# Kernel optimization log

Hardware: AMD Instinct MI355X
Metric: run time of the kernel (lower is better)

Reference implementation:

```python
import jax, jax.numpy as jnp
import numpy as np

B, S, D, H, C = 64, 512, 768, 768, 5


def setup_inputs() -> dict:
    key = jax.random.key(0)
    ks = jax.random.split(key, 7)
    return {
        "hidden_states": jax.random.normal(ks[0], (B, S, D), jnp.float32),
        "mask": jnp.ones((B, S), dtype=bool),
        # Dense(hidden_size, relu)
        "W1": jax.random.normal(ks[1], (D, H), jnp.float32) * 0.02,
        "b1": jnp.zeros((H,), jnp.float32),
        # CRF inner dense -> potentials over num_classes
        "W2": jax.random.normal(ks[2], (H, C), jnp.float32) * 0.02,
        "b2": jnp.zeros((C,), jnp.float32),
        # CRF transition matrix and boundary energies (tfa use_boundary=True)
        "chain_kernel": jax.random.normal(ks[3], (C, C), jnp.float32) * 0.1,
        "left_boundary": jax.random.normal(ks[4], (C,), jnp.float32) * 0.1,
        "right_boundary": jax.random.normal(ks[5], (C,), jnp.float32) * 0.1,
    }


def viterbi_decode(potentials, trans):
    """potentials: [B,S,C], trans: [C,C] -> decoded tags [B,S] int32."""
    pot_t = jnp.swapaxes(potentials, 0, 1)  # [S,B,C]

    def fwd_step(alpha, pot):
        scores = alpha[:, :, None] + trans[None]      # [B,C_prev,C_cur]
        bp = jnp.argmax(scores, axis=1)               # [B,C]
        alpha = jnp.max(scores, axis=1) + pot         # [B,C]
        return alpha, bp

    alpha, bps = jax.lax.scan(fwd_step, pot_t[0], pot_t[1:])  # bps: [S-1,B,C]
    last = jnp.argmax(alpha, axis=-1).astype(jnp.int32)       # [B]

    def back_step(tag, bp):
        prev = jnp.take_along_axis(bp, tag[:, None], axis=1)[:, 0].astype(jnp.int32)
        return prev, prev

    _, tags = jax.lax.scan(back_step, last, bps, reverse=True)  # [S-1,B]
    decoded = jnp.concatenate([jnp.swapaxes(tags, 0, 1), last[:, None]], axis=1)
    return decoded


def reference(hidden_states, mask, W1, b1, W2, b2, chain_kernel,
              left_boundary, right_boundary):
    # Dense + ReLU (dropout is identity at inference / training=False)
    h = jax.nn.relu(jnp.einsum('bsd,dh->bsh', hidden_states, W1) + b1)
    # CRF inner dense -> unary potentials
    pot = jnp.einsum('bsh,hc->bsc', h, W2) + b2
    # boundary energies at first / last timestep (mask is full-length here)
    pot = pot.at[:, 0].add(left_boundary).at[:, -1].add(right_boundary)
    seq_length = jnp.sum(mask.astype(jnp.int32), axis=1)
    decoded = viterbi_decode(pot, chain_kernel)
    return decoded, pot, seq_length, chain_kernel
```

## Files before the change

kernel.cpp:

```cpp
#include <hip/hip_runtime.h>

#define B_  64
#define S_  512
#define D_  768
#define H_  768
#define C_  5
#define M_  (B_ * S_)

typedef float f32x4 __attribute__((ext_vector_type(4)));
typedef short short8 __attribute__((ext_vector_type(8)));

#define W1T_ELEMS (D_ * H_)

__device__ __forceinline__ unsigned short f2bf(float f) {
    unsigned int u = __float_as_uint(f);
    u += 0x7FFFu + ((u >> 16) & 1u);
    return (unsigned short)(u >> 16);
}

__device__ __forceinline__ void gload16(const void* g, void* l) {
    __builtin_amdgcn_global_load_lds(
        (const __attribute__((address_space(1))) unsigned int*)g,
        (__attribute__((address_space(3))) unsigned int*)l, 16, 0, 0);
}

__global__ __launch_bounds__(256) void prep_w1_kernel(
    const float* __restrict__ W1, unsigned short* __restrict__ w1t)
{
    __shared__ float t[32][33];
    const int bx = blockIdx.x, by = blockIdx.y;
    const int lx = threadIdx.x & 31, ly = threadIdx.x >> 5;
    #pragma unroll
    for (int j = 0; j < 4; ++j)
        t[ly + 8 * j][lx] = W1[(by * 32 + ly + 8 * j) * H_ + bx * 32 + lx];
    __syncthreads();
    #pragma unroll
    for (int j = 0; j < 4; ++j)
        w1t[(size_t)(bx * 32 + ly + 8 * j) * D_ + by * 32 + lx] = f2bf(t[lx][ly + 8 * j]);
}

__global__ __launch_bounds__(256) void init_pot_kernel(
    const float* __restrict__ b2, const float* __restrict__ lb,
    const float* __restrict__ rb, float* __restrict__ pot)
{
    const int idx = blockIdx.x * 256 + threadIdx.x;
    if (idx < M_ * C_) {
        const int c = idx % C_;
        const int t = (idx / C_) & (S_ - 1);
        float v = b2[c];
        if (t == 0)      v += lb[c];
        if (t == S_ - 1) v += rb[c];
        pot[idx] = v;
    }
}

__global__ __launch_bounds__(512, 2) void gemm_fulln_kernel(
    const float* __restrict__ X,
    const unsigned short* __restrict__ w1t,
    const float* __restrict__ b1,
    const float* __restrict__ W2,
    const float* __restrict__ b2,
    const float* __restrict__ lb,
    const float* __restrict__ rb,
    float* __restrict__ pot)
{
    __shared__ __align__(16) unsigned short Alds[4 * 2 * 512];
    __shared__ __align__(16) unsigned short Blds[48 * 2 * 512];

    const int tid  = threadIdx.x;
    const int lane = tid & 63, w = tid >> 6;
    const int i15  = lane & 15, quad = lane >> 4;
    const int m0   = blockIdx.x * 64;

    const int arow = tid >> 3;
    const int ak0  = (tid & 7) * 8;
    const float* aSrc = X + (size_t)(m0 + arow) * D_ + ak0;
    unsigned short* aDst = &Alds[((arow >> 4) * 2 + (ak0 >> 5)) * 512
                                 + ((ak0 >> 3) & 3) * 128 + (arow & 15) * 8];

    const unsigned short* bSrc = w1t + (size_t)(6 * w * 16 + i15) * D_ + quad * 8;

    f32x4 acc[4][6];
    #pragma unroll
    for (int mi = 0; mi < 4; ++mi)
        #pragma unroll
        for (int ni = 0; ni < 6; ++ni)
            acc[mi][ni] = (f32x4){0.f, 0.f, 0.f, 0.f};

    #define STAGE(KB) do {                                                   \
        _Pragma("unroll")                                                    \
        for (int gi = 0; gi < 6; ++gi) {                                     \
            const unsigned short* s = bSrc + (size_t)gi * 16 * D_ + (KB);    \
            gload16(s,      &Blds[((6 * w + gi) * 2 + 0) * 512]);            \
            gload16(s + 32, &Blds[((6 * w + gi) * 2 + 1) * 512]);            \
        }                                                                    \
        {                                                                    \
            const float4 x0 = *(const float4*)(aSrc + (KB));                 \
            const float4 x1 = *(const float4*)(aSrc + (KB) + 4);             \
            union { unsigned short u[8]; uint4 v; } o;                       \
            o.u[0] = f2bf(x0.x); o.u[1] = f2bf(x0.y);                        \
            o.u[2] = f2bf(x0.z); o.u[3] = f2bf(x0.w);                        \
            o.u[4] = f2bf(x1.x); o.u[5] = f2bf(x1.y);                        \
            o.u[6] = f2bf(x1.z); o.u[7] = f2bf(x1.w);                        \
            *(uint4*)aDst = o.v;                                             \
        }                                                                    \
    } while (0)

    STAGE(0);
    #define KSTEPS (D_ / 64)
    for (int kt = 0; kt < KSTEPS; ++kt) {
        __syncthreads();

        #pragma unroll
        for (int kh = 0; kh < 2; ++kh) {
            short8 af[4], bfr[6];
            #pragma unroll
            for (int mi = 0; mi < 4; ++mi)
                af[mi] = *(const short8*)&Alds[(mi * 2 + kh) * 512 + lane * 8];
            #pragma unroll
            for (int ni = 0; ni < 6; ++ni)
                bfr[ni] = *(const short8*)&Blds[((w * 6 + ni) * 2 + kh) * 512 + lane * 8];
            #pragma unroll
            for (int ni = 0; ni < 6; ++ni)
                #pragma unroll
                for (int mi = 0; mi < 4; ++mi)
                    acc[mi][ni] = __builtin_amdgcn_mfma_f32_16x16x32_bf16(
                        af[mi], bfr[ni], acc[mi][ni], 0, 0, 0);
        }

        if (kt + 1 < KSTEPS) {
            __syncthreads();
            STAGE((kt + 1) * 64);
        }
    }
    __syncthreads();

    float* pp = (float*)&Blds[0];

    float b1v[6], w2v[6][C_];
    #pragma unroll
    for (int ni = 0; ni < 6; ++ni) {
        const int col = w * 96 + ni * 16 + i15;
        b1v[ni] = b1[col];
        #pragma unroll
        for (int cc = 0; cc < C_; ++cc) w2v[ni][cc] = W2[col * C_ + cc];
    }

    #pragma unroll
    for (int mi = 0; mi < 4; ++mi) {
        float ps[4][C_];
        #pragma unroll
        for (int r = 0; r < 4; ++r)
            #pragma unroll
            for (int cc = 0; cc < C_; ++cc) ps[r][cc] = 0.f;

        #pragma unroll
        for (int ni = 0; ni < 6; ++ni)
            #pragma unroll
            for (int r = 0; r < 4; ++r) {
                float h = acc[mi][ni][r] + b1v[ni];
                h = h > 0.f ? h : 0.f;
                #pragma unroll
                for (int cc = 0; cc < C_; ++cc)
                    ps[r][cc] = fmaf(h, w2v[ni][cc], ps[r][cc]);
            }

        #pragma unroll
        for (int off = 1; off < 16; off <<= 1)
            #pragma unroll
            for (int r = 0; r < 4; ++r)
                #pragma unroll
                for (int cc = 0; cc < C_; ++cc)
                    ps[r][cc] += __shfl_xor(ps[r][cc], off, 64);

        if (i15 == 0) {
            #pragma unroll
            for (int r = 0; r < 4; ++r) {
                const int row = mi * 16 + quad * 4 + r;
                #pragma unroll
                for (int cc = 0; cc < C_; ++cc)
                    pp[(w * 64 + row) * C_ + cc] = ps[r][cc];
            }
        }
    }
    __syncthreads();

    for (int idx = tid; idx < 64 * C_; idx += 512) {
        const int row = idx / C_, cc = idx % C_;
        float s = b2[cc];
        #pragma unroll
        for (int wv = 0; wv < 8; ++wv)
            s += pp[(wv * 64 + row) * C_ + cc];
        const int gm = m0 + row;
        const int tt = gm & (S_ - 1);
        if (tt == 0)      s += lb[cc];
        if (tt == S_ - 1) s += rb[cc];
        pot[(size_t)gm * C_ + cc] = s;
    }
}

#define FBK 8
#define FLDS 132
__global__ __launch_bounds__(256) void gemm_relu_pot_kernel(
    const float* __restrict__ X, const float* __restrict__ W1,
    const float* __restrict__ b1, const float* __restrict__ W2,
    float* __restrict__ pot)
{
    __shared__ float As[FBK * FLDS];
    __shared__ float Bs[FBK * FLDS];
    __shared__ float w2s[128][C_];

    const int tid = threadIdx.x;
    const int tx = tid & 15, ty = tid >> 4;
    const int m0 = blockIdx.y * 128, n0 = blockIdx.x * 128;

    for (int idx = tid; idx < 128 * C_; idx += 256)
        w2s[idx / C_][idx % C_] = W2[(n0 + idx / C_) * C_ + idx % C_];

    float acc[2][2][4][4];
    #pragma unroll
    for (int a = 0; a < 2; ++a)
        #pragma unroll
        for (int b = 0; b < 2; ++b)
            #pragma unroll
            for (int i = 0; i < 4; ++i)
                #pragma unroll
                for (int j = 0; j < 4; ++j) acc[a][b][i][j] = 0.f;

    const int arow = tid >> 1, aq = tid & 1;
    const int brow = tid >> 5, bq = tid & 31;
    const float* Aptr = X + (m0 + arow) * D_ + aq * 4;
    const float* Bptr = W1 + brow * H_ + n0 + bq * 4;

    for (int kt = 0; kt < D_; kt += FBK) {
        const float4 avv = *(const float4*)Aptr;
        const float4 bvv = *(const float4*)Bptr;
        __syncthreads();
        As[(aq * 4 + 0) * FLDS + arow] = avv.x;
        As[(aq * 4 + 1) * FLDS + arow] = avv.y;
        As[(aq * 4 + 2) * FLDS + arow] = avv.z;
        As[(aq * 4 + 3) * FLDS + arow] = avv.w;
        *(float4*)&Bs[brow * FLDS + bq * 4] = bvv;
        __syncthreads();
        #pragma unroll
        for (int k = 0; k < FBK; ++k) {
            const float4 a0 = *(const float4*)&As[k * FLDS + (ty << 2)];
            const float4 a1 = *(const float4*)&As[k * FLDS + 64 + (ty << 2)];
            const float4 b0 = *(const float4*)&Bs[k * FLDS + (tx << 2)];
            const float4 b1r = *(const float4*)&Bs[k * FLDS + 64 + (tx << 2)];
            const float ar[2][4] = {{a0.x,a0.y,a0.z,a0.w},{a1.x,a1.y,a1.z,a1.w}};
            const float br[2][4] = {{b0.x,b0.y,b0.z,b0.w},{b1r.x,b1r.y,b1r.z,b1r.w}};
            #pragma unroll
            for (int ri = 0; ri < 2; ++ri)
                #pragma unroll
                for (int i = 0; i < 4; ++i)
                    #pragma unroll
                    for (int rj = 0; rj < 2; ++rj)
                        #pragma unroll
                        for (int j = 0; j < 4; ++j)
                            acc[ri][rj][i][j] = fmaf(ar[ri][i], br[rj][j], acc[ri][rj][i][j]);
        }
        Aptr += FBK;
        Bptr += FBK * H_;
    }

    float ps[2][4][C_];
    #pragma unroll
    for (int ri = 0; ri < 2; ++ri)
        #pragma unroll
        for (int i = 0; i < 4; ++i)
            #pragma unroll
            for (int cc = 0; cc < C_; ++cc) ps[ri][i][cc] = 0.f;

    #pragma unroll
    for (int rj = 0; rj < 2; ++rj)
        #pragma unroll
        for (int j = 0; j < 4; ++j) {
            const int nl = rj * 64 + (tx << 2) + j;
            const float bj = b1[n0 + nl];
            float w2c[C_];
            #pragma unroll
            for (int cc = 0; cc < C_; ++cc) w2c[cc] = w2s[nl][cc];
            #pragma unroll
            for (int ri = 0; ri < 2; ++ri)
                #pragma unroll
                for (int i = 0; i < 4; ++i) {
                    float h = acc[ri][rj][i][j] + bj;
                    h = h > 0.f ? h : 0.f;
                    #pragma unroll
                    for (int cc = 0; cc < C_; ++cc)
                        ps[ri][i][cc] = fmaf(h, w2c[cc], ps[ri][i][cc]);
                }
        }

    #pragma unroll
    for (int off = 1; off < 16; off <<= 1)
        #pragma unroll
        for (int ri = 0; ri < 2; ++ri)
            #pragma unroll
            for (int i = 0; i < 4; ++i)
                #pragma unroll
                for (int cc = 0; cc < C_; ++cc)
                    ps[ri][i][cc] += __shfl_xor(ps[ri][i][cc], off, 64);

    if (tx == 0)
        #pragma unroll
        for (int ri = 0; ri < 2; ++ri)
            #pragma unroll
            for (int i = 0; i < 4; ++i) {
                const int m = m0 + ri * 64 + (ty << 2) + i;
                #pragma unroll
                for (int cc = 0; cc < C_; ++cc)
                    atomicAdd(&pot[m * C_ + cc], ps[ri][i][cc]);
            }
}

__global__ __launch_bounds__(64) void viterbi_kernel(
    const float* __restrict__ pot, const float* __restrict__ trans,
    const int* __restrict__ mask, float* __restrict__ decoded,
    float* __restrict__ seqlen, float* __restrict__ chain_out)
{
    const int b = blockIdx.x;
    const int lane = threadIdx.x;

    __shared__ float pl[S_ * C_];
    __shared__ unsigned int bpk[S_];
    __shared__ unsigned int gseg[64];
    __shared__ int bt[64];
    __shared__ int dec_s[S_];
    __shared__ int s_last;

    const float* pb = pot + b * (S_ * C_);
    for (int i = lane; i < S_ * C_; i += 64) pl[i] = pb[i];

    int mcnt = 0;
    const int* mb = mask + b * S_;
    for (int i = lane; i < S_; i += 64) mcnt += (mb[i] != 0) ? 1 : 0;
    #pragma unroll
    for (int off = 32; off >= 1; off >>= 1) mcnt += __shfl_xor(mcnt, off, 64);

    if (b == 0 && lane < C_ * C_) chain_out[lane] = trans[lane];

    float tr[C_][C_];
    #pragma unroll
    for (int p = 0; p < C_; ++p)
        #pragma unroll
        for (int c = 0; c < C_; ++c) tr[p][c] = trans[p * C_ + c];

    __syncthreads();

    const float NEG = -1.0e30f;

    float G[C_][C_];
    #pragma unroll
    for (int c = 0; c < C_; ++c)
        #pragma unroll
        for (int p = 0; p < C_; ++p) G[c][p] = (c == p) ? 0.f : NEG;

    for (int j = 1; j <= 8; ++j) {
        const int t = 8 * lane + j;
        if (t < S_) {
            float ng[C_][C_];
            #pragma unroll
            for (int c = 0; c < C_; ++c) {
                const float pc = pl[t * C_ + c];
                #pragma unroll
                for (int p = 0; p < C_; ++p) {
                    float m = tr[0][c] + G[0][p];
                    #pragma unroll
                    for (int q = 1; q < C_; ++q)
                        m = fmaxf(m, tr[q][c] + G[q][p]);
                    ng[c][p] = m + pc;
                }
            }
            #pragma unroll
            for (int c = 0; c < C_; ++c)
                #pragma unroll
                for (int p = 0; p < C_; ++p) G[c][p] = ng[c][p];
        }
    }

    #pragma unroll
    for (int d = 1; d < 64; d <<= 1) {
        float Q[C_][C_];
        #pragma unroll
        for (int q = 0; q < C_; ++q)
            #pragma unroll
            for (int p = 0; p < C_; ++p) Q[q][p] = __shfl_up(G[q][p], d, 64);
        if (lane >= d) {
            float ng[C_][C_];
            #pragma unroll
            for (int c = 0; c < C_; ++c)
                #pragma unroll
                for (int p = 0; p < C_; ++p) {
                    float m = G[c][0] + Q[0][p];
                    #pragma unroll
                    for (int q = 1; q < C_; ++q)
                        m = fmaxf(m, G[c][q] + Q[q][p]);
                    ng[c][p] = m;
                }
            #pragma unroll
            for (int c = 0; c < C_; ++c)
                #pragma unroll
                for (int p = 0; p < C_; ++p) G[c][p] = ng[c][p];
        }
    }

    float a[C_];
    {
        float E[C_][C_];
        #pragma unroll
        for (int c = 0; c < C_; ++c)
            #pragma unroll
            for (int p = 0; p < C_; ++p) E[c][p] = __shfl_up(G[c][p], 1, 64);
        float a0[C_];
        #pragma unroll
        for (int c = 0; c < C_; ++c) a0[c] = pl[c];
        if (lane == 0) {
            #pragma unroll
            for (int c = 0; c < C_; ++c) a[c] = a0[c];
        } else {
            #pragma unroll
            for (int c = 0; c < C_; ++c) {
                float m = E[c][0] + a0[0];
                #pragma unroll
                for (int q = 1; q < C_; ++q) m = fmaxf(m, E[c][q] + a0[q]);
                a[c] = m;
            }
        }
    }

    for (int j = 1; j <= 8; ++j) {
        const int t = 8 * lane + j;
        if (t < S_) {
            unsigned int mpack = 0;
            float na[C_];
            #pragma unroll
            for (int c = 0; c < C_; ++c) {
                float best = a[0] + tr[0][c];
                int arg = 0;
                #pragma unroll
                for (int p = 1; p < C_; ++p) {
                    const float s = a[p] + tr[p][c];
                    if (s > best) { best = s; arg = p; }
                }
                mpack |= (unsigned int)arg << (3 * c);
                na[c] = best + pl[t * C_ + c];
            }
            bpk[t] = mpack;
            #pragma unroll
            for (int c = 0; c < C_; ++c) a[c] = na[c];
        }
    }

    if (lane == 63) {
        float best = a[0];
        int arg = 0;
        #pragma unroll
        for (int p = 1; p < C_; ++p)
            if (a[p] > best) { best = a[p]; arg = p; }
        s_last = arg;
    }
    if (lane == 0) bpk[0] = 0;
    __syncthreads();

    const int last = s_last;

    unsigned int g = 0u | (1u << 3) | (2u << 6) | (3u << 9) | (4u << 12);
    #pragma unroll
    for (int j = 7; j >= 0; --j) {
        const int t = 8 * lane + j;
        if (t >= 1) {
            const unsigned int m = bpk[t];
            unsigned int ng = 0;
            #pragma unroll
            for (int x = 0; x < C_; ++x) {
                const unsigned int gx = (g >> (3 * x)) & 7u;
                ng |= ((m >> (3 * gx)) & 7u) << (3 * x);
            }
            g = ng;
        }
    }
    gseg[lane] = g;
    __syncthreads();

    if (lane == 0) {
        int cur = last;
        for (int l = 63; l >= 0; --l) {
            bt[l] = cur;
            cur = (int)((gseg[l] >> (3 * cur)) & 7u);
        }
        seqlen[b] = (float)mcnt;
    }
    __syncthreads();

    {
        int tag = bt[lane];
        const int t0 = 8 * lane;
        dec_s[t0 + 7] = tag;
        #pragma unroll
        for (int t = t0 + 7; t >= t0 + 1; --t) {
            tag = (int)((bpk[t] >> (3 * tag)) & 7u);
            dec_s[t - 1] = tag;
        }
    }
    __syncthreads();

    float* db = decoded + b * S_;
    for (int i = lane; i < S_; i += 64) db[i] = (float)dec_s[i];
}

extern "C" void kernel_launch(void* const* d_in, const int* in_sizes, int n_in,
                              void* d_out, int out_size, void* d_ws, size_t ws_size,
                              hipStream_t stream) {
    const float* hs    = (const float*)d_in[0];
    const int*   mask  = (const int*)  d_in[1];
    const float* W1    = (const float*)d_in[2];
    const float* b1    = (const float*)d_in[3];
    const float* W2    = (const float*)d_in[4];
    const float* b2    = (const float*)d_in[5];
    const float* chain = (const float*)d_in[6];
    const float* lb    = (const float*)d_in[7];
    const float* rb    = (const float*)d_in[8];

    float* out      = (float*)d_out;
    float* decoded  = out;
    float* pot      = out + M_;
    float* seq      = out + M_ + M_ * C_;
    float* chainout = seq + B_;

    const size_t need_w1 = (size_t)W1T_ELEMS * sizeof(unsigned short);

    if (ws_size >= need_w1) {
        unsigned short* w1t = (unsigned short*)d_ws;
        dim3 pgrid(H_ / 32, D_ / 32);
        prep_w1_kernel<<<pgrid, 256, 0, stream>>>(W1, w1t);
        gemm_fulln_kernel<<<M_ / 64, 512, 0, stream>>>(
            hs, w1t, b1, W2, b2, lb, rb, pot);
    } else {
        const int PI_BLOCKS = (M_ * C_ + 255) / 256;
        init_pot_kernel<<<PI_BLOCKS, 256, 0, stream>>>(b2, lb, rb, pot);
        dim3 grid(H_ / 128, M_ / 128);
        gemm_relu_pot_kernel<<<grid, 256, 0, stream>>>(hs, W1, b1, W2, pot);
    }

    viterbi_kernel<<<B_, 64, 0, stream>>>(pot, chain, mask, decoded, seq, chainout);
}
```

Measured before the change: 271.4 us.

## Pre-convert X to bf16 and make a W1-slice-resident GEMM with atomic potential reduction

Adds a combined prep kernel that converts all of X to bf16 in workspace, transposes W1 to bf16 and initializes the potentials with the bias and boundary terms. The GEMM is restructured so each block keeps a 96-column slice of W1 entirely in LDS across K and streams 1024 rows of A straight from global memory into registers, with no per-k-step LDS staging or barriers. Partial potentials over the N slices are combined with float atomicAdd into pot. This removes the repeated W1 traffic and the in-loop A conversion, at the cost of an extra bf16 write and read of X, atomic contention, and summation order that is no longer deterministic.

Measured after the change: 516.7 us. 1.9x slower.

```diff
diff --git a/kernel.cpp b/kernel.cpp
--- a/kernel.cpp
+++ b/kernel.cpp
@@ -11,6 +11,11 @@
 typedef short short8 __attribute__((ext_vector_type(8)));
 
 #define W1T_ELEMS (D_ * H_)
+#define XBF_ELEMS (M_ * D_)
+
+#define PX_BLOCKS   (XBF_ELEMS / (256 * 8))
+#define PW_BLOCKS   ((D_ / 32) * (H_ / 32))
+#define PI_BLOCKS   ((M_ * C_ + 255) / 256)
 
 __device__ __forceinline__ unsigned short f2bf(float f) {
     unsigned int u = __float_as_uint(f);
@@ -24,19 +29,48 @@
         (__attribute__((address_space(3))) unsigned int*)l, 16, 0, 0);
 }
 
-__global__ __launch_bounds__(256) void prep_w1_kernel(
-    const float* __restrict__ W1, unsigned short* __restrict__ w1t)
+__global__ __launch_bounds__(256) void prep_all_kernel(
+    const float* __restrict__ X, const float* __restrict__ W1,
+    const float* __restrict__ b2, const float* __restrict__ lb,
+    const float* __restrict__ rb,
+    unsigned short* __restrict__ xbf, unsigned short* __restrict__ w1t,
+    float* __restrict__ pot)
 {
     __shared__ float t[32][33];
-    const int bx = blockIdx.x, by = blockIdx.y;
-    const int lx = threadIdx.x & 31, ly = threadIdx.x >> 5;
-    #pragma unroll
-    for (int j = 0; j < 4; ++j)
-        t[ly + 8 * j][lx] = W1[(by * 32 + ly + 8 * j) * H_ + bx * 32 + lx];
-    __syncthreads();
-    #pragma unroll
-    for (int j = 0; j < 4; ++j)
-        w1t[(size_t)(bx * 32 + ly + 8 * j) * D_ + by * 32 + lx] = f2bf(t[lx][ly + 8 * j]);
+    const int bid = blockIdx.x;
+    const int tid = threadIdx.x;
+
+    if (bid < PX_BLOCKS) {
+        const size_t i0 = ((size_t)bid * 256 + tid) * 8;
+        const float4 a = *(const float4*)(X + i0);
+        const float4 b = *(const float4*)(X + i0 + 4);
+        union { unsigned short u[8]; uint4 v; } o;
+        o.u[0] = f2bf(a.x); o.u[1] = f2bf(a.y); o.u[2] = f2bf(a.z); o.u[3] = f2bf(a.w);
+        o.u[4] = f2bf(b.x); o.u[5] = f2bf(b.y); o.u[6] = f2bf(b.z); o.u[7] = f2bf(b.w);
+        *(uint4*)(xbf + i0) = o.v;
+    } else if (bid < PX_BLOCKS + PW_BLOCKS) {
+        const int b2i = bid - PX_BLOCKS;
+        const int bx = b2i % (H_ / 32);
+        const int by = b2i / (H_ / 32);
+        const int lx = tid & 31, ly = tid >> 5;
+        #pragma unroll
+        for (int j = 0; j < 4; ++j)
+            t[ly + 8 * j][lx] = W1[(by * 32 + ly + 8 * j) * H_ + bx * 32 + lx];
+        __syncthreads();
+        #pragma unroll
+        for (int j = 0; j < 4; ++j)
+            w1t[(size_t)(bx * 32 + ly + 8 * j) * D_ + by * 32 + lx] = f2bf(t[lx][ly + 8 * j]);
+    } else {
+        const int idx = (bid - PX_BLOCKS - PW_BLOCKS) * 256 + tid;
+        if (idx < M_ * C_) {
+            const int c = idx % C_;
+            const int tt = (idx / C_) & (S_ - 1);
+            float v = b2[c];
+            if (tt == 0)      v += lb[c];
+            if (tt == S_ - 1) v += rb[c];
+            pot[idx] = v;
+        }
+    }
 }
 
 __global__ __launch_bounds__(256) void init_pot_kernel(
@@ -54,148 +88,122 @@
     }
 }
 
-__global__ __launch_bounds__(512, 2) void gemm_fulln_kernel(
-    const float* __restrict__ X,
+#define NS_   8
+#define NCOL_ 96
+#define KF_   (D_ / 32)
+
+__global__ __launch_bounds__(512, 2) void gemm_nres_kernel(
+    const unsigned short* __restrict__ xbf,
     const unsigned short* __restrict__ w1t,
     const float* __restrict__ b1,
     const float* __restrict__ W2,
-    const float* __restrict__ b2,
-    const float* __restrict__ lb,
-    const float* __restrict__ rb,
     float* __restrict__ pot)
 {
-    __shared__ __align__(16) unsigned short Alds[4 * 2 * 512];
-    __shared__ __align__(16) unsigned short Blds[48 * 2 * 512];
+    __shared__ __align__(16) unsigned short Blds[KF_ * 6 * 512];
+    __shared__ float W2s[NCOL_ * C_];
+    __shared__ float B1s[NCOL_];
 
     const int tid  = threadIdx.x;
     const int lane = tid & 63, w = tid >> 6;
     const int i15  = lane & 15, quad = lane >> 4;
-    const int m0   = blockIdx.x * 64;
-
-    const int arow = tid >> 3;
-    const int ak0  = (tid & 7) * 8;
-    const float* aSrc = X + (size_t)(m0 + arow) * D_ + ak0;
-    unsigned short* aDst = &Alds[((arow >> 4) * 2 + (ak0 >> 5)) * 512
-                                 + ((ak0 >> 3) & 3) * 128 + (arow & 15) * 8];
-
-    const unsigned short* bSrc = w1t + (size_t)(6 * w * 16 + i15) * D_ + quad * 8;
-
-    f32x4 acc[4][6];
-    #pragma unroll
-    for (int mi = 0; mi < 4; ++mi)
-        #pragma unroll
-        for (int ni = 0; ni < 6; ++ni)
-            acc[mi][ni] = (f32x4){0.f, 0.f, 0.f, 0.f};
-
-    #define STAGE(KB) do {                                                   \
-        _Pragma("unroll")                                                    \
-        for (int gi = 0; gi < 6; ++gi) {                                     \
-            const unsigned short* s = bSrc + (size_t)gi * 16 * D_ + (KB);    \
-            gload16(s,      &Blds[((6 * w + gi) * 2 + 0) * 512]);            \
-            gload16(s + 32, &Blds[((6 * w + gi) * 2 + 1) * 512]);            \
-        }                                                                    \
-        {                                                                    \
-            const float4 x0 = *(const float4*)(aSrc + (KB));                 \
-            const float4 x1 = *(const float4*)(aSrc + (KB) + 4);             \
-            union { unsigned short u[8]; uint4 v; } o;                       \
-            o.u[0] = f2bf(x0.x); o.u[1] = f2bf(x0.y);                        \
-            o.u[2] = f2bf(x0.z); o.u[3] = f2bf(x0.w);                        \
-            o.u[4] = f2bf(x1.x); o.u[5] = f2bf(x1.y);                        \
-            o.u[6] = f2bf(x1.z); o.u[7] = f2bf(x1.w);                        \
-            *(uint4*)aDst = o.v;                                             \
-        }                                                                    \
-    } while (0)
-
-    STAGE(0);
-    #define KSTEPS (D_ / 64)
-    for (int kt = 0; kt < KSTEPS; ++kt) {
-        __syncthreads();
-
-        #pragma unroll
-        for (int kh = 0; kh < 2; ++kh) {
-            short8 af[4], bfr[6];
-            #pragma unroll
-            for (int mi = 0; mi < 4; ++mi)
-                af[mi] = *(const short8*)&Alds[(mi * 2 + kh) * 512 + lane * 8];
+
+    const int bid  = blockIdx.x;
+    const int ns   = bid >> 5;
+    const int mgrp = bid & 31;
+    const int n0   = ns * NCOL_;
+
+    #pragma unroll
+    for (int j = 0; j < 18; ++j) {
+        const int idx = w * 18 + j;
+        const int kf = idx / 6, g = idx % 6;
+        const unsigned short* src =
+            w1t + (size_t)(n0 + g * 16 + i15) * D_ + kf * 32 + quad * 8;
+        gload16(src, &Blds[idx * 512]);
+    }
+    if (tid < NCOL_ * C_) W2s[tid] = W2[(n0 + tid / C_) * C_ + tid % C_];
+    else if (tid < NCOL_ * C_ + NCOL_) B1s[tid - NCOL_ * C_] = b1[n0 + tid - NCOL_ * C_];
+    __syncthreads();
+
+    for (int c = 0; c < 4; ++c) {
+        const int rowb = mgrp * 1024 + c * 256 + w * 32;
+
+        f32x4 acc[2][6];
+        #pragma unroll
+        for (int mi = 0; mi < 2; ++mi)
             #pragma unroll
             for (int ni = 0; ni < 6; ++ni)
-                bfr[ni] = *(const short8*)&Blds[((w * 6 + ni) * 2 + kh) * 512 + lane * 8];
-            #pragma unroll
-            for (int ni = 0; ni < 6; ++ni)
-                #pragma unroll
-                for (int mi = 0; mi < 4; ++mi)
-                    acc[mi][ni] = __builtin_amdgcn_mfma_f32_16x16x32_bf16(
-                        af[mi], bfr[ni], acc[mi][ni], 0, 0, 0);
-        }
-
-        if (kt + 1 < KSTEPS) {
-            __syncthreads();
-            STAGE((kt + 1) * 64);
-        }
-    }
-    __syncthreads();
-
-    float* pp = (float*)&Blds[0];
-
-    float b1v[6], w2v[6][C_];
-    #pragma unroll
-    for (int ni = 0; ni < 6; ++ni) {
-        const int col = w * 96 + ni * 16 + i15;
-        b1v[ni] = b1[col];
-        #pragma unroll
-        for (int cc = 0; cc < C_; ++cc) w2v[ni][cc] = W2[col * C_ + cc];
-    }
-
-    #pragma unroll
-    for (int mi = 0; mi < 4; ++mi) {
-        float ps[4][C_];
-        #pragma unroll
-        for (int r = 0; r < 4; ++r)
-            #pragma unroll
-            for (int cc = 0; cc < C_; ++cc) ps[r][cc] = 0.f;
-
-        #pragma unroll
-        for (int ni = 0; ni < 6; ++ni)
-            #pragma unroll
-            for (int r = 0; r < 4; ++r) {
-                float h = acc[mi][ni][r] + b1v[ni];
-                h = h > 0.f ? h : 0.f;
-                #pragma unroll
-                for (int cc = 0; cc < C_; ++cc)
-                    ps[r][cc] = fmaf(h, w2v[ni][cc], ps[r][cc]);
-            }
-
-        #pragma unroll
-        for (int off = 1; off < 16; off <<= 1)
+                acc[mi][ni] = (f32x4){0.f, 0.f, 0.f, 0.f};
+
+        const unsigned short* aRow0 = xbf + (size_t)(rowb + i15)      * D_ + quad * 8;
+        const unsigned short* aRow1 = xbf + (size_t)(rowb + 16 + i15) * D_ + quad * 8;
+
+        #pragma unroll
+        for (int h = 0; h < 2; ++h) {
+            short8 af[2][12];
+            #pragma unroll
+            for (int kf = 0; kf < 12; ++kf) {
+                af[0][kf] = *(const short8*)(aRow0 + h * 384 + kf * 32);
+                af[1][kf] = *(const short8*)(aRow1 + h * 384 + kf * 32);
+            }
+            #pragma unroll
+            for (int kf = 0; kf < 12; ++kf) {
+                short8 bfr[6];
+                #pragma unroll
+                for (int ni = 0; ni < 6; ++ni)
+                    bfr[ni] = *(const short8*)
+                        &Blds[((h * 12 + kf) * 6 + ni) * 512 + lane * 8];
+                #pragma unroll
+                for (int ni = 0; ni < 6; ++ni)
+                    #pragma unroll
+                    for (int mi = 0; mi < 2; ++mi)
+                        acc[mi][ni] = __builtin_amdgcn_mfma_f32_16x16x32_bf16(
+                            af[mi][kf], bfr[ni], acc[mi][ni], 0, 0, 0);
+            }
+        }
+
+        #pragma unroll
+        for (int mi = 0; mi < 2; ++mi) {
+            float ps[4][C_];
             #pragma unroll
             for (int r = 0; r < 4; ++r)
                 #pragma unroll
-                for (int cc = 0; cc < C_; ++cc)
-                    ps[r][cc] += __shfl_xor(ps[r][cc], off, 64);
-
-        if (i15 == 0) {
-            #pragma unroll
-            for (int r = 0; r < 4; ++r) {
-                const int row = mi * 16 + quad * 4 + r;
-                #pragma unroll
-                for (int cc = 0; cc < C_; ++cc)
-                    pp[(w * 64 + row) * C_ + cc] = ps[r][cc];
-            }
-        }
-    }
-    __syncthreads();
-
-    for (int idx = tid; idx < 64 * C_; idx += 512) {
-        const int row = idx / C_, cc = idx % C_;
-        float s = b2[cc];
-        #pragma unroll
-        for (int wv = 0; wv < 8; ++wv)
-            s += pp[(wv * 64 + row) * C_ + cc];
-        const int gm = m0 + row;
-        const int tt = gm & (S_ - 1);
-        if (tt == 0)      s += lb[cc];
-        if (tt == S_ - 1) s += rb[cc];
-        pot[(size_t)gm * C_ + cc] = s;
+                for (int cc = 0; cc < C_; ++cc) ps[r][cc] = 0.f;
+
+            #pragma unroll
+            for (int ni = 0; ni < 6; ++ni) {
+                const int colL = ni * 16 + i15;
+                const float b1v = B1s[colL];
+                float w2v[C_];
+                #pragma unroll
+                for (int cc = 0; cc < C_; ++cc) w2v[cc] = W2s[colL * C_ + cc];
+                #pragma unroll
+                for (int r = 0; r < 4; ++r) {
+                    float hh = acc[mi][ni][r] + b1v;
+                    hh = hh > 0.f ? hh : 0.f;
+                    #pragma unroll
+                    for (int cc = 0; cc < C_; ++cc)
+                        ps[r][cc] = fmaf(hh, w2v[cc], ps[r][cc]);
+                }
+            }
+
+            #pragma unroll
+            for (int off = 1; off < 16; off <<= 1)
+                #pragma unroll
+                for (int r = 0; r < 4; ++r)
+                    #pragma unroll
+                    for (int cc = 0; cc < C_; ++cc)
+                        ps[r][cc] += __shfl_xor(ps[r][cc], off, 64);
+
+            if (i15 == 0) {
+                #pragma unroll
+                for (int r = 0; r < 4; ++r) {
+                    const int row = rowb + mi * 16 + quad * 4 + r;
+                    #pragma unroll
+                    for (int cc = 0; cc < C_; ++cc)
+                        atomicAdd(&pot[(size_t)row * C_ + cc], ps[r][cc]);
+                }
+            }
+        }
     }
 }
 
@@ -529,16 +537,16 @@
     float* seq      = out + M_ + M_ * C_;
     float* chainout = seq + B_;
 
-    const size_t need_w1 = (size_t)W1T_ELEMS * sizeof(unsigned short);
-
-    if (ws_size >= need_w1) {
+    const size_t need_all = (size_t)W1T_ELEMS * sizeof(unsigned short)
+                          + (size_t)XBF_ELEMS * sizeof(unsigned short);
+
+    if (ws_size >= need_all) {
         unsigned short* w1t = (unsigned short*)d_ws;
-        dim3 pgrid(H_ / 32, D_ / 32);
-        prep_w1_kernel<<<pgrid, 256, 0, stream>>>(W1, w1t);
-        gemm_fulln_kernel<<<M_ / 64, 512, 0, stream>>>(
-            hs, w1t, b1, W2, b2, lb, rb, pot);
+        unsigned short* xbf = w1t + W1T_ELEMS;
+        prep_all_kernel<<<PX_BLOCKS + PW_BLOCKS + PI_BLOCKS, 256, 0, stream>>>(
+            hs, W1, b2, lb, rb, xbf, w1t, pot);
+        gemm_nres_kernel<<<256, 512, 0, stream>>>(xbf, w1t, b1, W2, pot);
     } else {
-        const int PI_BLOCKS = (M_ * C_ + 255) / 256;
         init_pot_kernel<<<PI_BLOCKS, 256, 0, stream>>>(b2, lb, rb, pot);
         dim3 grid(H_ / 128, M_ / 128);
         gemm_relu_pot_kernel<<<grid, 256, 0, stream>>>(hs, W1, b1, W2, pot);
```

## Pre-convert X to bf16 and keep full-K A tile resident in LDS

Applied to the files above, without the earlier changes.

A prep kernel now converts the whole activation matrix to bf16 in the workspace alongside the W1 transpose. The GEMM then loads its 64-row by 768-K A tile into LDS once via global_load_lds, and reads W1 fragments directly from global/L2 into registers instead of staging them through LDS. This removes the per-K-step syncs and in-loop conversion. In exchange it adds an extra full pass over X (fp32 read plus bf16 write and reread), lowers occupancy to one block per CU, and leaves B loads unstaged from global with no software pipelining.

After: 286.5 us. 5.5% more time.

```diff
diff --git a/kernel.cpp b/kernel.cpp
--- a/kernel.cpp
+++ b/kernel.cpp
@@ -11,6 +11,10 @@
 typedef short short8 __attribute__((ext_vector_type(8)));
 
 #define W1T_ELEMS (D_ * H_)
+#define XBF_ELEMS (M_ * D_)
+
+#define PX_BLOCKS   (XBF_ELEMS / (256 * 8))
+#define PW_BLOCKS   ((D_ / 32) * (H_ / 32))
 
 __device__ __forceinline__ unsigned short f2bf(float f) {
     unsigned int u = __float_as_uint(f);
@@ -24,19 +28,35 @@
         (__attribute__((address_space(3))) unsigned int*)l, 16, 0, 0);
 }
 
-__global__ __launch_bounds__(256) void prep_w1_kernel(
-    const float* __restrict__ W1, unsigned short* __restrict__ w1t)
+__global__ __launch_bounds__(256) void prep_all_kernel(
+    const float* __restrict__ X, const float* __restrict__ W1,
+    unsigned short* __restrict__ xbf, unsigned short* __restrict__ w1t)
 {
     __shared__ float t[32][33];
-    const int bx = blockIdx.x, by = blockIdx.y;
-    const int lx = threadIdx.x & 31, ly = threadIdx.x >> 5;
-    #pragma unroll
-    for (int j = 0; j < 4; ++j)
-        t[ly + 8 * j][lx] = W1[(by * 32 + ly + 8 * j) * H_ + bx * 32 + lx];
-    __syncthreads();
-    #pragma unroll
-    for (int j = 0; j < 4; ++j)
-        w1t[(size_t)(bx * 32 + ly + 8 * j) * D_ + by * 32 + lx] = f2bf(t[lx][ly + 8 * j]);
+    const int bid = blockIdx.x;
+    const int tid = threadIdx.x;
+
+    if (bid < PX_BLOCKS) {
+        const size_t i0 = ((size_t)bid * 256 + tid) * 8;
+        const float4 a = *(const float4*)(X + i0);
+        const float4 b = *(const float4*)(X + i0 + 4);
+        union { unsigned short u[8]; uint4 v; } o;
+        o.u[0] = f2bf(a.x); o.u[1] = f2bf(a.y); o.u[2] = f2bf(a.z); o.u[3] = f2bf(a.w);
+        o.u[4] = f2bf(b.x); o.u[5] = f2bf(b.y); o.u[6] = f2bf(b.z); o.u[7] = f2bf(b.w);
+        *(uint4*)(xbf + i0) = o.v;
+    } else {
+        const int b2i = bid - PX_BLOCKS;
+        const int bx = b2i % (H_ / 32);
+        const int by = b2i / (H_ / 32);
+        const int lx = tid & 31, ly = tid >> 5;
+        #pragma unroll
+        for (int j = 0; j < 4; ++j)
+            t[ly + 8 * j][lx] = W1[(by * 32 + ly + 8 * j) * H_ + bx * 32 + lx];
+        __syncthreads();
+        #pragma unroll
+        for (int j = 0; j < 4; ++j)
+            w1t[(size_t)(bx * 32 + ly + 8 * j) * D_ + by * 32 + lx] = f2bf(t[lx][ly + 8 * j]);
+    }
 }
 
 __global__ __launch_bounds__(256) void init_pot_kernel(
@@ -54,8 +74,8 @@
     }
 }
 
-__global__ __launch_bounds__(512, 2) void gemm_fulln_kernel(
-    const float* __restrict__ X,
+__global__ __launch_bounds__(512, 1) void gemm_ares_kernel(
+    const unsigned short* __restrict__ xbf,
     const unsigned short* __restrict__ w1t,
     const float* __restrict__ b1,
     const float* __restrict__ W2,
@@ -64,21 +84,27 @@
     const float* __restrict__ rb,
     float* __restrict__ pot)
 {
-    __shared__ __align__(16) unsigned short Alds[4 * 2 * 512];
-    __shared__ __align__(16) unsigned short Blds[48 * 2 * 512];
+    __shared__ __align__(16) unsigned short Alds[4 * 24 * 512];
 
     const int tid  = threadIdx.x;
     const int lane = tid & 63, w = tid >> 6;
     const int i15  = lane & 15, quad = lane >> 4;
-    const int m0   = blockIdx.x * 64;
-
-    const int arow = tid >> 3;
-    const int ak0  = (tid & 7) * 8;
-    const float* aSrc = X + (size_t)(m0 + arow) * D_ + ak0;
-    unsigned short* aDst = &Alds[((arow >> 4) * 2 + (ak0 >> 5)) * 512
-                                 + ((ak0 >> 3) & 3) * 128 + (arow & 15) * 8];
-
-    const unsigned short* bSrc = w1t + (size_t)(6 * w * 16 + i15) * D_ + quad * 8;
+    const int rowb = blockIdx.x * 64;
+
+    #pragma unroll
+    for (int j = 0; j < 12; ++j) {
+        const int idx = w * 12 + j;
+        const int g = idx / 24, kf = idx % 24;
+        const unsigned short* src =
+            xbf + (size_t)(rowb + g * 16 + i15) * D_ + kf * 32 + quad * 8;
+        gload16(src, &Alds[idx * 512]);
+    }
+    __syncthreads();
+
+    const unsigned short* bw[6];
+    #pragma unroll
+    for (int ni = 0; ni < 6; ++ni)
+        bw[ni] = w1t + (size_t)(w * 96 + ni * 16 + i15) * D_ + quad * 8;
 
     f32x4 acc[4][6];
     #pragma unroll
@@ -87,55 +113,22 @@
         for (int ni = 0; ni < 6; ++ni)
             acc[mi][ni] = (f32x4){0.f, 0.f, 0.f, 0.f};
 
-    #define STAGE(KB) do {                                                   \
-        _Pragma("unroll")                                                    \
-        for (int gi = 0; gi < 6; ++gi) {                                     \
-            const unsigned short* s = bSrc + (size_t)gi * 16 * D_ + (KB);    \
-            gload16(s,      &Blds[((6 * w + gi) * 2 + 0) * 512]);            \
-            gload16(s + 32, &Blds[((6 * w + gi) * 2 + 1) * 512]);            \
-        }                                                                    \
-        {                                                                    \
-            const float4 x0 = *(const float4*)(aSrc + (KB));                 \
-            const float4 x1 = *(const float4*)(aSrc + (KB) + 4);             \
-            union { unsigned short u[8]; uint4 v; } o;                       \
-            o.u[0] = f2bf(x0.x); o.u[1] = f2bf(x0.y);                        \
-            o.u[2] = f2bf(x0.z); o.u[3] = f2bf(x0.w);                        \
-            o.u[4] = f2bf(x1.x); o.u[5] = f2bf(x1.y);                        \
-            o.u[6] = f2bf(x1.z); o.u[7] = f2bf(x1.w);                        \
-            *(uint4*)aDst = o.v;                                             \
-        }                                                                    \
-    } while (0)
-
-    STAGE(0);
-    #define KSTEPS (D_ / 64)
-    for (int kt = 0; kt < KSTEPS; ++kt) {
-        __syncthreads();
-
-        #pragma unroll
-        for (int kh = 0; kh < 2; ++kh) {
-            short8 af[4], bfr[6];
+    #pragma unroll
+    for (int kf = 0; kf < 24; ++kf) {
+        short8 bfr[6], af[4];
+        #pragma unroll
+        for (int ni = 0; ni < 6; ++ni)
+            bfr[ni] = *(const short8*)(bw[ni] + kf * 32);
+        #pragma unroll
+        for (int mi = 0; mi < 4; ++mi)
+            af[mi] = *(const short8*)&Alds[(mi * 24 + kf) * 512 + lane * 8];
+        #pragma unroll
+        for (int ni = 0; ni < 6; ++ni)
             #pragma unroll
             for (int mi = 0; mi < 4; ++mi)
-                af[mi] = *(const short8*)&Alds[(mi * 2 + kh) * 512 + lane * 8];
-            #pragma unroll
-            for (int ni = 0; ni < 6; ++ni)
-                bfr[ni] = *(const short8*)&Blds[((w * 6 + ni) * 2 + kh) * 512 + lane * 8];
-            #pragma unroll
-            for (int ni = 0; ni < 6; ++ni)
-                #pragma unroll
-                for (int mi = 0; mi < 4; ++mi)
-                    acc[mi][ni] = __builtin_amdgcn_mfma_f32_16x16x32_bf16(
-                        af[mi], bfr[ni], acc[mi][ni], 0, 0, 0);
-        }
-
-        if (kt + 1 < KSTEPS) {
-            __syncthreads();
-            STAGE((kt + 1) * 64);
-        }
-    }
-    __syncthreads();
-
-    float* pp = (float*)&Blds[0];
+                acc[mi][ni] = __builtin_amdgcn_mfma_f32_16x16x32_bf16(
+                    af[mi], bfr[ni], acc[mi][ni], 0, 0, 0);
+    }
 
     float b1v[6], w2v[6][C_];
     #pragma unroll
@@ -146,6 +139,9 @@
         for (int cc = 0; cc < C_; ++cc) w2v[ni][cc] = W2[col * C_ + cc];
     }
 
+    __syncthreads();
+    float* pp = (float*)&Alds[0];
+
     #pragma unroll
     for (int mi = 0; mi < 4; ++mi) {
         float ps[4][C_];
@@ -158,11 +154,11 @@
         for (int ni = 0; ni < 6; ++ni)
             #pragma unroll
             for (int r = 0; r < 4; ++r) {
-                float h = acc[mi][ni][r] + b1v[ni];
-                h = h > 0.f ? h : 0.f;
+                float hh = acc[mi][ni][r] + b1v[ni];
+                hh = hh > 0.f ? hh : 0.f;
                 #pragma unroll
                 for (int cc = 0; cc < C_; ++cc)
-                    ps[r][cc] = fmaf(h, w2v[ni][cc], ps[r][cc]);
+                    ps[r][cc] = fmaf(hh, w2v[ni][cc], ps[r][cc]);
             }
 
         #pragma unroll
@@ -191,7 +187,7 @@
         #pragma unroll
         for (int wv = 0; wv < 8; ++wv)
             s += pp[(wv * 64 + row) * C_ + cc];
-        const int gm = m0 + row;
+        const int gm = rowb + row;
         const int tt = gm & (S_ - 1);
         if (tt == 0)      s += lb[cc];
         if (tt == S_ - 1) s += rb[cc];
@@ -529,17 +525,17 @@
     float* seq      = out + M_ + M_ * C_;
     float* chainout = seq + B_;
 
-    const size_t need_w1 = (size_t)W1T_ELEMS * sizeof(unsigned short);
-
-    if (ws_size >= need_w1) {
+    const size_t need_bf = (size_t)W1T_ELEMS * 2 + (size_t)XBF_ELEMS * 2;
+
+    if (ws_size >= need_bf) {
         unsigned short* w1t = (unsigned short*)d_ws;
-        dim3 pgrid(H_ / 32, D_ / 32);
-        prep_w1_kernel<<<pgrid, 256, 0, stream>>>(W1, w1t);
-        gemm_fulln_kernel<<<M_ / 64, 512, 0, stream>>>(
-            hs, w1t, b1, W2, b2, lb, rb, pot);
+        unsigned short* xbf = w1t + W1T_ELEMS;
+        prep_all_kernel<<<PX_BLOCKS + PW_BLOCKS, 256, 0, stream>>>(
+            hs, W1, xbf, w1t);
+        gemm_ares_kernel<<<M_ / 64, 512, 0, stream>>>(
+            xbf, w1t, b1, W2, b2, lb, rb, pot);
     } else {
-        const int PI_BLOCKS = (M_ * C_ + 255) / 256;
-        init_pot_kernel<<<PI_BLOCKS, 256, 0, stream>>>(b2, lb, rb, pot);
+        init_pot_kernel<<<(M_ * C_ + 255) / 256, 256, 0, stream>>>(b2, lb, rb, pot);
         dim3 grid(H_ / 128, M_ / 128);
         gemm_relu_pot_kernel<<<grid, 256, 0, stream>>>(hs, W1, b1, W2, pot);
     }
```

## Split GEMM across N halves with register-direct B loads and partial reduction

Applied to the files above, without the earlier changes.

The fused GEMM now gives each block a 128-row by 384-column tile instead of 64 rows by all 768 columns. B fragments are loaded straight from global memory into registers, dropping the LDS staging for B. The bf16 conversion of A is double-buffered in LDS, with the next tile's global loads prefetched during the MFMA work. Because each block covers only half the columns, the two column halves write partial potentials to workspace and a new reduce kernel sums them and adds the bias and boundary terms. This trades the larger LDS footprint and the B-tile barrier for more global B traffic, an extra launch, and an extra pass over the partial buffers.

New measurement: 255.6 us. -5.8%, faster.

```diff
diff --git a/kernel.cpp b/kernel.cpp
--- a/kernel.cpp
+++ b/kernel.cpp
@@ -11,17 +11,12 @@
 typedef short short8 __attribute__((ext_vector_type(8)));
 
 #define W1T_ELEMS (D_ * H_)
+#define PART2_ELEMS (2 * M_ * C_)
 
 __device__ __forceinline__ unsigned short f2bf(float f) {
     unsigned int u = __float_as_uint(f);
     u += 0x7FFFu + ((u >> 16) & 1u);
     return (unsigned short)(u >> 16);
-}
-
-__device__ __forceinline__ void gload16(const void* g, void* l) {
-    __builtin_amdgcn_global_load_lds(
-        (const __attribute__((address_space(1))) unsigned int*)g,
-        (__attribute__((address_space(3))) unsigned int*)l, 16, 0, 0);
 }
 
 __global__ __launch_bounds__(256) void prep_w1_kernel(
@@ -54,100 +49,113 @@
     }
 }
 
-__global__ __launch_bounds__(512, 2) void gemm_fulln_kernel(
+__global__ __launch_bounds__(512) void gemm_half_kernel(
     const float* __restrict__ X,
     const unsigned short* __restrict__ w1t,
     const float* __restrict__ b1,
     const float* __restrict__ W2,
-    const float* __restrict__ b2,
-    const float* __restrict__ lb,
-    const float* __restrict__ rb,
-    float* __restrict__ pot)
+    float* __restrict__ part)
 {
-    __shared__ __align__(16) unsigned short Alds[4 * 2 * 512];
-    __shared__ __align__(16) unsigned short Blds[48 * 2 * 512];
+    __shared__ __align__(16) unsigned short At[2][8192];
+    __shared__ float pp[8][128][C_];
 
     const int tid  = threadIdx.x;
     const int lane = tid & 63, w = tid >> 6;
     const int i15  = lane & 15, quad = lane >> 4;
-    const int m0   = blockIdx.x * 64;
-
-    const int arow = tid >> 3;
-    const int ak0  = (tid & 7) * 8;
-    const float* aSrc = X + (size_t)(m0 + arow) * D_ + ak0;
-    unsigned short* aDst = &Alds[((arow >> 4) * 2 + (ak0 >> 5)) * 512
-                                 + ((ak0 >> 3) & 3) * 128 + (arow & 15) * 8];
-
-    const unsigned short* bSrc = w1t + (size_t)(6 * w * 16 + i15) * D_ + quad * 8;
-
-    f32x4 acc[4][6];
-    #pragma unroll
-    for (int mi = 0; mi < 4; ++mi)
-        #pragma unroll
-        for (int ni = 0; ni < 6; ++ni)
+
+    const int bid  = blockIdx.x;
+    const int nh   = bid & 1;
+    const int rg   = bid >> 1;
+    const int rowb = rg * 128;
+    const int ncol0 = nh * 384 + w * 48;
+
+    const unsigned short* bw[3];
+    #pragma unroll
+    for (int ni = 0; ni < 3; ++ni)
+        bw[ni] = w1t + (size_t)(ncol0 + ni * 16 + i15) * D_ + quad * 8;
+
+    const int arow = tid >> 2;
+    const int ak4  = tid & 3;
+    const float* aSrc = X + (size_t)(rowb + arow) * D_ + ak4 * 16;
+    const int o0 = ak4 * 2, o1 = ak4 * 2 + 1;
+    const int dst0 = ((arow >> 4) * 2 + (o0 >> 2)) * 512 + ((o0 & 3) * 16 + (arow & 15)) * 8;
+    const int dst1 = ((arow >> 4) * 2 + (o1 >> 2)) * 512 + ((o1 & 3) * 16 + (arow & 15)) * 8;
+
+    f32x4 acc[8][3];
+    #pragma unroll
+    for (int mi = 0; mi < 8; ++mi)
+        #pragma unroll
+        for (int ni = 0; ni < 3; ++ni)
             acc[mi][ni] = (f32x4){0.f, 0.f, 0.f, 0.f};
 
-    #define STAGE(KB) do {                                                   \
-        _Pragma("unroll")                                                    \
-        for (int gi = 0; gi < 6; ++gi) {                                     \
-            const unsigned short* s = bSrc + (size_t)gi * 16 * D_ + (KB);    \
-            gload16(s,      &Blds[((6 * w + gi) * 2 + 0) * 512]);            \
-            gload16(s + 32, &Blds[((6 * w + gi) * 2 + 1) * 512]);            \
-        }                                                                    \
-        {                                                                    \
-            const float4 x0 = *(const float4*)(aSrc + (KB));                 \
-            const float4 x1 = *(const float4*)(aSrc + (KB) + 4);             \
-            union { unsigned short u[8]; uint4 v; } o;                       \
-            o.u[0] = f2bf(x0.x); o.u[1] = f2bf(x0.y);                        \
-            o.u[2] = f2bf(x0.z); o.u[3] = f2bf(x0.w);                        \
-            o.u[4] = f2bf(x1.x); o.u[5] = f2bf(x1.y);                        \
-            o.u[6] = f2bf(x1.z); o.u[7] = f2bf(x1.w);                        \
-            *(uint4*)aDst = o.v;                                             \
-        }                                                                    \
-    } while (0)
-
-    STAGE(0);
-    #define KSTEPS (D_ / 64)
-    for (int kt = 0; kt < KSTEPS; ++kt) {
-        __syncthreads();
+    {
+        const float4 xa = *(const float4*)(aSrc);
+        const float4 xb = *(const float4*)(aSrc + 4);
+        const float4 xc = *(const float4*)(aSrc + 8);
+        const float4 xd = *(const float4*)(aSrc + 12);
+        union { unsigned short u[8]; uint4 v; } p, q;
+        p.u[0] = f2bf(xa.x); p.u[1] = f2bf(xa.y); p.u[2] = f2bf(xa.z); p.u[3] = f2bf(xa.w);
+        p.u[4] = f2bf(xb.x); p.u[5] = f2bf(xb.y); p.u[6] = f2bf(xb.z); p.u[7] = f2bf(xb.w);
+        q.u[0] = f2bf(xc.x); q.u[1] = f2bf(xc.y); q.u[2] = f2bf(xc.z); q.u[3] = f2bf(xc.w);
+        q.u[4] = f2bf(xd.x); q.u[5] = f2bf(xd.y); q.u[6] = f2bf(xd.z); q.u[7] = f2bf(xd.w);
+        *(uint4*)&At[0][dst0] = p.v;
+        *(uint4*)&At[0][dst1] = q.v;
+    }
+    __syncthreads();
+
+    for (int kt = 0; kt < 12; ++kt) {
+        const int cur = kt & 1;
+        const bool pre = (kt < 11);
+
+        float4 xa, xb, xc, xd;
+        if (pre) {
+            const float* s = aSrc + (kt + 1) * 64;
+            xa = *(const float4*)(s);
+            xb = *(const float4*)(s + 4);
+            xc = *(const float4*)(s + 8);
+            xd = *(const float4*)(s + 12);
+        }
 
         #pragma unroll
         for (int kh = 0; kh < 2; ++kh) {
-            short8 af[4], bfr[6];
-            #pragma unroll
-            for (int mi = 0; mi < 4; ++mi)
-                af[mi] = *(const short8*)&Alds[(mi * 2 + kh) * 512 + lane * 8];
-            #pragma unroll
-            for (int ni = 0; ni < 6; ++ni)
-                bfr[ni] = *(const short8*)&Blds[((w * 6 + ni) * 2 + kh) * 512 + lane * 8];
-            #pragma unroll
-            for (int ni = 0; ni < 6; ++ni)
-                #pragma unroll
-                for (int mi = 0; mi < 4; ++mi)
+            short8 af[8], bfr[3];
+            #pragma unroll
+            for (int mi = 0; mi < 8; ++mi)
+                af[mi] = *(const short8*)&At[cur][(mi * 2 + kh) * 512 + lane * 8];
+            #pragma unroll
+            for (int ni = 0; ni < 3; ++ni)
+                bfr[ni] = *(const short8*)(bw[ni] + kt * 64 + kh * 32);
+            #pragma unroll
+            for (int ni = 0; ni < 3; ++ni)
+                #pragma unroll
+                for (int mi = 0; mi < 8; ++mi)
                     acc[mi][ni] = __builtin_amdgcn_mfma_f32_16x16x32_bf16(
                         af[mi], bfr[ni], acc[mi][ni], 0, 0, 0);
         }
 
-        if (kt + 1 < KSTEPS) {
-            __syncthreads();
-            STAGE((kt + 1) * 64);
-        }
-    }
-    __syncthreads();
-
-    float* pp = (float*)&Blds[0];
-
-    float b1v[6], w2v[6][C_];
-    #pragma unroll
-    for (int ni = 0; ni < 6; ++ni) {
-        const int col = w * 96 + ni * 16 + i15;
+        if (pre) {
+            union { unsigned short u[8]; uint4 v; } p, q;
+            p.u[0] = f2bf(xa.x); p.u[1] = f2bf(xa.y); p.u[2] = f2bf(xa.z); p.u[3] = f2bf(xa.w);
+            p.u[4] = f2bf(xb.x); p.u[5] = f2bf(xb.y); p.u[6] = f2bf(xb.z); p.u[7] = f2bf(xb.w);
+            q.u[0] = f2bf(xc.x); q.u[1] = f2bf(xc.y); q.u[2] = f2bf(xc.z); q.u[3] = f2bf(xc.w);
+            q.u[4] = f2bf(xd.x); q.u[5] = f2bf(xd.y); q.u[6] = f2bf(xd.z); q.u[7] = f2bf(xd.w);
+            *(uint4*)&At[cur ^ 1][dst0] = p.v;
+            *(uint4*)&At[cur ^ 1][dst1] = q.v;
+        }
+        __syncthreads();
+    }
+
+    float b1v[3], w2v[3][C_];
+    #pragma unroll
+    for (int ni = 0; ni < 3; ++ni) {
+        const int col = ncol0 + ni * 16 + i15;
         b1v[ni] = b1[col];
         #pragma unroll
         for (int cc = 0; cc < C_; ++cc) w2v[ni][cc] = W2[col * C_ + cc];
     }
 
     #pragma unroll
-    for (int mi = 0; mi < 4; ++mi) {
+    for (int mi = 0; mi < 8; ++mi) {
         float ps[4][C_];
         #pragma unroll
         for (int r = 0; r < 4; ++r)
@@ -155,14 +163,14 @@
             for (int cc = 0; cc < C_; ++cc) ps[r][cc] = 0.f;
 
         #pragma unroll
-        for (int ni = 0; ni < 6; ++ni)
+        for (int ni = 0; ni < 3; ++ni)
             #pragma unroll
             for (int r = 0; r < 4; ++r) {
-                float h = acc[mi][ni][r] + b1v[ni];
-                h = h > 0.f ? h : 0.f;
+                float hh = acc[mi][ni][r] + b1v[ni];
+                hh = hh > 0.f ? hh : 0.f;
                 #pragma unroll
                 for (int cc = 0; cc < C_; ++cc)
-                    ps[r][cc] = fmaf(h, w2v[ni][cc], ps[r][cc]);
+                    ps[r][cc] = fmaf(hh, w2v[ni][cc], ps[r][cc]);
             }
 
         #pragma unroll
@@ -179,23 +187,36 @@
                 const int row = mi * 16 + quad * 4 + r;
                 #pragma unroll
                 for (int cc = 0; cc < C_; ++cc)
-                    pp[(w * 64 + row) * C_ + cc] = ps[r][cc];
-            }
-        }
-    }
-    __syncthreads();
-
-    for (int idx = tid; idx < 64 * C_; idx += 512) {
+                    pp[w][row][cc] = ps[r][cc];
+            }
+        }
+    }
+    __syncthreads();
+
+    for (int idx = tid; idx < 128 * C_; idx += 512) {
         const int row = idx / C_, cc = idx % C_;
-        float s = b2[cc];
+        float s = 0.f;
         #pragma unroll
         for (int wv = 0; wv < 8; ++wv)
-            s += pp[(wv * 64 + row) * C_ + cc];
-        const int gm = m0 + row;
-        const int tt = gm & (S_ - 1);
-        if (tt == 0)      s += lb[cc];
-        if (tt == S_ - 1) s += rb[cc];
-        pot[(size_t)gm * C_ + cc] = s;
+            s += pp[wv][row][cc];
+        part[((size_t)nh * M_ + rowb + row) * C_ + cc] = s;
+    }
+}
+
+__global__ __launch_bounds__(256) void reduce_pot_kernel(
+    const float* __restrict__ part, const float* __restrict__ b2,
+    const float* __restrict__ lb, const float* __restrict__ rb,
+    float* __restrict__ pot)
+{
+    const int idx = blockIdx.x * 256 + threadIdx.x;
+    if (idx < M_ * C_) {
+        const int c = idx % C_;
+        const int t = (idx / C_) & (S_ - 1);
+        float v = b2[c];
+        if (t == 0)      v += lb[c];
+        if (t == S_ - 1) v += rb[c];
+        v += part[idx] + part[(size_t)(M_ * C_) + idx];
+        pot[idx] = v;
     }
 }
 
@@ -529,17 +550,18 @@
     float* seq      = out + M_ + M_ * C_;
     float* chainout = seq + B_;
 
-    const size_t need_w1 = (size_t)W1T_ELEMS * sizeof(unsigned short);
-
-    if (ws_size >= need_w1) {
+    const size_t need = (size_t)W1T_ELEMS * 2 + (size_t)PART2_ELEMS * 4;
+
+    if (ws_size >= need) {
         unsigned short* w1t = (unsigned short*)d_ws;
+        float* part = (float*)(w1t + W1T_ELEMS);
         dim3 pgrid(H_ / 32, D_ / 32);
         prep_w1_kernel<<<pgrid, 256, 0, stream>>>(W1, w1t);
-        gemm_fulln_kernel<<<M_ / 64, 512, 0, stream>>>(
-            hs, w1t, b1, W2, b2, lb, rb, pot);
+        gemm_half_kernel<<<512, 512, 0, stream>>>(hs, w1t, b1, W2, part);
+        reduce_pot_kernel<<<(M_ * C_ + 255) / 256, 256, 0, stream>>>(
+            part, b2, lb, rb, pot);
     } else {
-        const int PI_BLOCKS = (M_ * C_ + 255) / 256;
-        init_pot_kernel<<<PI_BLOCKS, 256, 0, stream>>>(b2, lb, rb, pot);
+        init_pot_kernel<<<(M_ * C_ + 255) / 256, 256, 0, stream>>>(b2, lb, rb, pot);
         dim3 grid(H_ / 128, M_ / 128);
         gemm_relu_pot_kernel<<<grid, 256, 0, stream>>>(hs, W1, b1, W2, pot);
     }
```
